# Kernel optimization log

Measured on AMD Instinct MI355X. Metric: run time of the kernel, lower is better.

Reference implementation:

```python
import jax, jax.numpy as jnp
import numpy as np

N = 8192      # nodes
NIN = 128     # input feature dim
NH = 128      # hidden dim
NC = 8        # communities
CS = N // NC  # community size


def setup_inputs() -> dict:
    key = jax.random.key(0)
    k = jax.random.split(key, 6)
    seq1 = jax.random.normal(k[0], (1, N, NIN), jnp.float32)
    seq2 = jax.random.normal(k[1], (1, N, NIN), jnp.float32)
    # dense row-stochastic-ish adjacency so GCN activations stay O(1)
    adj = jax.random.uniform(k[2], (1, N, N), jnp.float32) * (2.0 / N)
    cc_label = jnp.arange(N, dtype=jnp.int32).reshape(NC, CS)  # partition of nodes
    W = jax.random.normal(k[3], (NIN, NH), jnp.float32) / np.float32(np.sqrt(NIN))
    b = jnp.zeros((NH,), jnp.float32)
    Wb = jax.random.normal(k[4], (NH, NH), jnp.float32) / np.float32(np.sqrt(NH))
    bb = jnp.zeros((), jnp.float32)
    return {"seq1": seq1, "seq2": seq2, "adj": adj, "cc_label": cc_label,
            "W": W, "b": b, "Wb": Wb, "bb": bb}


def reference(seq1, seq2, adj, cc_label, W, b, Wb, bb):
    def gcn(seq):
        fts = jnp.einsum('bnd,dh->bnh', seq, W)            # linear
        agg = jnp.einsum('bnm,bmh->bnh', adj, fts) + b     # neighborhood aggregation
        return jax.nn.relu(agg)

    h1 = gcn(seq1)[0]   # [N, NH]
    h2 = gcn(seq2)[0]   # [N, NH]

    # ragged per-community gather (communities are equal-size here)
    hg1 = h1[cc_label]  # [NC, CS, NH]
    hg2 = h2[cc_label]  # [NC, CS, NH]

    # AvgReadout (msk=None) + sigmoid -> per-community summary
    c = jax.nn.sigmoid(jnp.mean(hg1, axis=1))              # [NC, NH]

    # Discriminator: bilinear f_k(h, c) = h @ Wb @ c + bb
    cw = jnp.einsum('hk,nk->nh', Wb, c)                    # [NC, NH]
    sc1 = jnp.einsum('nch,nh->nc', hg1, cw) + bb           # [NC, CS]
    sc2 = jnp.einsum('nch,nh->nc', hg2, cw) + bb           # [NC, CS]

    # scalar scatter-back (each node written exactly once)
    flat = cc_label.reshape(-1)
    ret1 = jnp.zeros((N,), h1.dtype).at[flat].set(sc1.reshape(-1))
    ret2 = jnp.zeros((N,), h2.dtype).at[flat].set(sc2.reshape(-1))
    return jnp.concatenate([ret1, ret2])[None, :]          # [1, 2N]
```

## Files before the change

### kernel.cpp

```cpp
#include <hip/hip_runtime.h>


#define NN    8192
#define NCOLS 256
#define ASCALE 4096.0f
#define AINV  (1.0f/4096.0f)

typedef _Float16 half8 __attribute__((ext_vector_type(8)));
typedef float    f32x4 __attribute__((ext_vector_type(4)));

#define VMCNT(n) asm volatile("s_waitcnt vmcnt(" #n ")" ::: "memory")

__device__ __forceinline__ void gload16(const void* g, void* l) {
  __builtin_amdgcn_global_load_lds(
      (const __attribute__((address_space(1))) char*)g,
      (__attribute__((address_space(3))) char*)l, 16, 0, 0);
}

__global__ void k0_init(const int* __restrict__ cc, int* __restrict__ node_comm,
                        float* __restrict__ S) {
  int i = blockIdx.x * 256 + threadIdx.x;
  if (i < 1024) S[i] = 0.0f;
  node_comm[cc[i]] = i >> 10;
}

__global__ __launch_bounds__(256) void k1_fts(const float* __restrict__ seq1,
                                              const float* __restrict__ seq2,
                                              const float* __restrict__ W,
                                              _Float16* __restrict__ F) {
  __shared__ char lds[65536];
  _Float16* Wt  = (_Float16*)lds;
  float*    sSeq = (float*)(lds + 32768);
  const int tid = threadIdx.x;
  const int lane = tid & 63;
  const int w = tid >> 6;
  const int l15 = lane & 15;
  const int g = lane >> 4;
  const int m0 = blockIdx.x * 64;

  for (int it = 0; it < 64; ++it) {
    int idx = it * 256 + tid;
    int d = idx >> 7, hc = idx & 127;
    int byte = (hc * 256 + d * 2) ^ ((hc & 7) << 4);
    *(_Float16*)(lds + byte) = (_Float16)W[idx];
  }

  const float* seqp[2] = {seq1, seq2};
  const int srow = tid >> 5;
  const int sck = tid & 31;

  for (int s = 0; s < 2; ++s) {
    __syncthreads();
    const float* sp = seqp[s];
#pragma unroll
    for (int i = 0; i < 8; ++i) {
      int row = i * 8 + srow;
      gload16(sp + (size_t)(m0 + row) * 128 + ((sck ^ (row & 7)) << 2),
              (char*)sSeq + i * 4096 + w * 1024);
    }
    asm volatile("s_waitcnt vmcnt(0)" ::: "memory");
    __syncthreads();

    f32x4 acc[4][2] = {};
    const float4* S4 = (const float4*)sSeq;
    const float4* W4 = (const float4*)Wt;
#pragma unroll
    for (int kk = 0; kk < 4; ++kk) {
      half8 bf[2];
#pragma unroll
      for (int nf = 0; nf < 2; ++nf) {
        int col = w * 32 + nf * 16 + l15;
        float4 bv = W4[(col * 16 + kk * 4 + g) ^ (col & 7)];
        bf[nf] = *(const half8*)&bv;
      }
#pragma unroll
      for (int mf = 0; mf < 4; ++mf) {
        int row = mf * 16 + l15;
        int bidx = row * 32 + kk * 8 + g * 2;
        float4 u = S4[bidx ^ (row & 7)];
        float4 v = S4[(bidx + 1) ^ (row & 7)];
        half8 af;
#pragma unroll
        for (int j = 0; j < 4; ++j) af[j] = (_Float16)(((const float*)&u)[j]);
#pragma unroll
        for (int j = 0; j < 4; ++j) af[4 + j] = (_Float16)(((const float*)&v)[j]);
#pragma unroll
        for (int nf = 0; nf < 2; ++nf)
          acc[mf][nf] = __builtin_amdgcn_mfma_f32_16x16x32_f16(af, bf[nf], acc[mf][nf], 0, 0, 0);
      }
    }
    __syncthreads();
    _Float16* img = (_Float16*)sSeq;
#pragma unroll
    for (int mf = 0; mf < 4; ++mf)
#pragma unroll
      for (int nf = 0; nf < 2; ++nf) {
        int col = w * 32 + nf * 16 + l15;
#pragma unroll
        for (int j = 0; j < 4; ++j) {
          int kl = mf * 16 + g * 4 + j;
          img[(kl >> 5) * 4096 + col * 32 + (kl & 31)] = (_Float16)acc[mf][nf][j];
        }
      }
    __syncthreads();
    const float4* src4 = (const float4*)sSeq;
#pragma unroll
    for (int i = 0; i < 4; ++i) {
      int e = i * 256 + tid;
      int kt = e >> 9, off = e & 511;
      ((float4*)(F + (size_t)(2 * blockIdx.x + kt) * 8192))[s * 512 + off] = src4[e];
    }
  }
}

__global__ __launch_bounds__(512) void k2_gemm(const float* __restrict__ adj,
                                               const _Float16* __restrict__ F,
                                               float* __restrict__ Pp) {
  __shared__ float    sA[3][4096];
  __shared__ _Float16 sB[3][8192];
  const int tid = threadIdx.x;
  const int lane = tid & 63;
  const int w = tid >> 6;
  const int l15 = lane & 15;
  const int g = lane >> 4;
  const int row0 = blockIdx.x * 128;
  const int ks = blockIdx.y;
  const int kcol0 = ks * 2048;

  const int ar0 = tid >> 3;
  const int ac = tid & 7;
  const float* asrc0 = adj + (size_t)(row0 + ar0) * NN + kcol0 + ((ac ^ (ar0 & 7)) << 2);
  const float* asrc1 = adj + (size_t)(row0 + ar0 + 64) * NN + kcol0 + ((ac ^ (ar0 & 7)) << 2);
  const char*  bsrc  = (const char*)F + (size_t)(ks * 64) * 16384 + (size_t)tid * 16;

  auto stage = [&](int buf, int t) {
    gload16(asrc0 + t * 32, (char*)sA[buf] + w * 1024);
    gload16(asrc1 + t * 32, (char*)sA[buf] + 8192 + w * 1024);
    const char* bs = bsrc + (size_t)t * 16384;
    gload16(bs,        (char*)sB[buf] + w * 1024);
    gload16(bs + 8192, (char*)sB[buf] + 8192 + w * 1024);
  };

  const int wm = w >> 2, wn = w & 3;
  f32x4 acc[4][4] = {};

  auto compute = [&](int buf) {
    const float4* A4 = (const float4*)sA[buf];
    const float4* B4 = (const float4*)sB[buf];
    half8 bf[4];
#pragma unroll
    for (int nf = 0; nf < 4; ++nf) {
      int col = wn * 64 + nf * 16 + l15;
      float4 bv = B4[col * 4 + g];
      bf[nf] = *(const half8*)&bv;
    }
#pragma unroll
    for (int mf = 0; mf < 4; ++mf) {
      int row = wm * 64 + mf * 16 + l15;
      int bidx = row * 8 + g * 2;
      float4 u = A4[bidx ^ (row & 7)];
      float4 v = A4[(bidx + 1) ^ (row & 7)];
      half8 af;
#pragma unroll
      for (int j = 0; j < 4; ++j) af[j] = (_Float16)(((const float*)&u)[j] * ASCALE);
#pragma unroll
      for (int j = 0; j < 4; ++j) af[4 + j] = (_Float16)(((const float*)&v)[j] * ASCALE);
#pragma unroll
      for (int nf = 0; nf < 4; ++nf)
        acc[mf][nf] = __builtin_amdgcn_mfma_f32_16x16x32_f16(af, bf[nf], acc[mf][nf], 0, 0, 0);
    }
  };

  stage(0, 0);
  stage(1, 1);
  stage(2, 2);
  int cur = 0;
  for (int t = 0; t < 61; ++t) {
    VMCNT(8);
    __builtin_amdgcn_s_barrier();
    compute(cur);
    __builtin_amdgcn_s_barrier();
    stage(cur, t + 3);
    cur = (cur == 2) ? 0 : cur + 1;
  }
  VMCNT(8); __builtin_amdgcn_s_barrier();
  compute(cur); cur = (cur == 2) ? 0 : cur + 1;
  VMCNT(4); __builtin_amdgcn_s_barrier();
  compute(cur); cur = (cur == 2) ? 0 : cur + 1;
  VMCNT(0); __builtin_amdgcn_s_barrier();
  compute(cur);

#pragma unroll
  for (int mf = 0; mf < 4; ++mf)
#pragma unroll
    for (int nf = 0; nf < 4; ++nf) {
      int col = wn * 64 + nf * 16 + l15;
#pragma unroll
      for (int j = 0; j < 4; ++j) {
        int row = row0 + wm * 64 + mf * 16 + g * 4 + j;
        Pp[((size_t)ks * NN + row) * NCOLS + col] = acc[mf][nf][j];
      }
    }
}

__global__ void k2r_reduce(const float* __restrict__ Pp, const float* __restrict__ b,
                           float* __restrict__ h) {
  int gid = blockIdx.x * 256 + threadIdx.x;
  size_t base = (size_t)gid * 4;
  float4 p0 = *(const float4*)(Pp + base);
  float4 p1 = *(const float4*)(Pp + base + 2097152);
  float4 p2 = *(const float4*)(Pp + base + 4194304);
  float4 p3 = *(const float4*)(Pp + base + 6291456);
  int n0 = (int)(base & 255) & 127;
  float4 r;
  r.x = fmaxf((p0.x + p1.x + p2.x + p3.x) * AINV + b[n0],     0.f);
  r.y = fmaxf((p0.y + p1.y + p2.y + p3.y) * AINV + b[n0 + 1], 0.f);
  r.z = fmaxf((p0.z + p1.z + p2.z + p3.z) * AINV + b[n0 + 2], 0.f);
  r.w = fmaxf((p0.w + p1.w + p2.w + p3.w) * AINV + b[n0 + 3], 0.f);
  *(float4*)(h + base) = r;
}

__global__ __launch_bounds__(128) void k3a_csum(const float* __restrict__ h,
                                                const int* __restrict__ node_comm,
                                                float* __restrict__ S) {
  int hh = threadIdx.x;
  int n0 = blockIdx.x * 32;
  float a0=0,a1=0,a2=0,a3=0,a4=0,a5=0,a6=0,a7=0;
  for (int i = 0; i < 32; ++i) {
    int node = n0 + i;
    int c = node_comm[node];
    float v = h[(size_t)node * 256 + hh];
    a0 += (c == 0) ? v : 0.f;  a1 += (c == 1) ? v : 0.f;
    a2 += (c == 2) ? v : 0.f;  a3 += (c == 3) ? v : 0.f;
    a4 += (c == 4) ? v : 0.f;  a5 += (c == 5) ? v : 0.f;
    a6 += (c == 6) ? v : 0.f;  a7 += (c == 7) ? v : 0.f;
  }
  if (a0 != 0.f) atomicAdd(&S[0 * 128 + hh], a0);
  if (a1 != 0.f) atomicAdd(&S[1 * 128 + hh], a1);
  if (a2 != 0.f) atomicAdd(&S[2 * 128 + hh], a2);
  if (a3 != 0.f) atomicAdd(&S[3 * 128 + hh], a3);
  if (a4 != 0.f) atomicAdd(&S[4 * 128 + hh], a4);
  if (a5 != 0.f) atomicAdd(&S[5 * 128 + hh], a5);
  if (a6 != 0.f) atomicAdd(&S[6 * 128 + hh], a6);
  if (a7 != 0.f) atomicAdd(&S[7 * 128 + hh], a7);
}

__global__ __launch_bounds__(128) void k3b_cw(const float* __restrict__ S,
                                              const float* __restrict__ Wb,
                                              float* __restrict__ cw) {
  __shared__ float sc[128];
  int ci = blockIdx.x;
  int hh = threadIdx.x;
  float m = S[ci * 128 + hh] * (1.0f / 1024.0f);
  sc[hh] = 1.0f / (1.0f + __expf(-m));
  __syncthreads();
  const float4* wr = (const float4*)(Wb + (size_t)hh * 128);
  float acc = 0.f;
#pragma unroll 8
  for (int k4 = 0; k4 < 32; ++k4) {
    float4 wv = wr[k4];
    acc += wv.x * sc[k4 * 4 + 0] + wv.y * sc[k4 * 4 + 1]
         + wv.z * sc[k4 * 4 + 2] + wv.w * sc[k4 * 4 + 3];
  }
  cw[ci * 128 + hh] = acc;
}

__global__ __launch_bounds__(256) void k5_score(const float* __restrict__ h,
                                                const int* __restrict__ node_comm,
                                                const float* __restrict__ cw,
                                                const float* __restrict__ bbp,
                                                float* __restrict__ out) {
  int tid = threadIdx.x;
  int q = tid & 15, nl = tid >> 4;
  int node = blockIdx.x * 16 + nl;
  int c = node_comm[node];
  const float* hr = h + (size_t)node * 256;
  const float* cr = cw + c * 128;
  float4 c0 = *(const float4*)(cr + q * 8);
  float4 c1 = *(const float4*)(cr + q * 8 + 4);
  float4 a0 = *(const float4*)(hr + q * 8);
  float4 a1 = *(const float4*)(hr + q * 8 + 4);
  float p1 = a0.x*c0.x + a0.y*c0.y + a0.z*c0.z + a0.w*c0.w
           + a1.x*c1.x + a1.y*c1.y + a1.z*c1.z + a1.w*c1.w;
  float4 b0 = *(const float4*)(hr + 128 + q * 8);
  float4 b1 = *(const float4*)(hr + 128 + q * 8 + 4);
  float p2 = b0.x*c0.x + b0.y*c0.y + b0.z*c0.z + b0.w*c0.w
           + b1.x*c1.x + b1.y*c1.y + b1.z*c1.z + b1.w*c1.w;
#pragma unroll
  for (int m = 8; m >= 1; m >>= 1) {
    p1 += __shfl_xor(p1, m, 64);
    p2 += __shfl_xor(p2, m, 64);
  }
  if (q == 0) {
    float bb = bbp[0];
    out[node] = p1 + bb;
    out[8192 + node] = p2 + bb;
  }
}

extern "C" void kernel_launch(void* const* d_in, const int* in_sizes, int n_in,
                              void* d_out, int out_size, void* d_ws, size_t ws_size,
                              hipStream_t stream) {
  (void)in_sizes; (void)n_in; (void)out_size; (void)ws_size;
  const float* seq1 = (const float*)d_in[0];
  const float* seq2 = (const float*)d_in[1];
  const float* adj  = (const float*)d_in[2];
  const int*   cc   = (const int*)d_in[3];
  const float* W    = (const float*)d_in[4];
  const float* b    = (const float*)d_in[5];
  const float* Wb   = (const float*)d_in[6];
  const float* bb   = (const float*)d_in[7];
  float* out = (float*)d_out;

  char* ws = (char*)d_ws;
  _Float16* F   = (_Float16*)(ws);
  float* h      = (float*)(ws + (4u << 20));
  float* Pp     = (float*)(ws + (12u << 20));
  float* S      = (float*)(ws + (44u << 20));
  float* cw     = (float*)(ws + (44u << 20) + 4096);
  int* node_comm = (int*)(ws + (44u << 20) + 8192);

  k0_init<<<dim3(32), dim3(256), 0, stream>>>(cc, node_comm, S);
  k1_fts<<<dim3(128), dim3(256), 0, stream>>>(seq1, seq2, W, F);
  k2_gemm<<<dim3(64, 4), dim3(512), 0, stream>>>(adj, F, Pp);
  k2r_reduce<<<dim3(2048), dim3(256), 0, stream>>>(Pp, b, h);
  k3a_csum<<<dim3(256), dim3(128), 0, stream>>>(h, node_comm, S);
  k3b_cw<<<dim3(8), dim3(128), 0, stream>>>(S, Wb, cw);
  k5_score<<<dim3(512), dim3(256), 0, stream>>>(h, node_comm, cw, bb, out);
}
```

Measured before the change: 128.9 us.

## Fuse split-K reduce, community summary, and scoring into one grid-synced tail kernel

The split-K reduction, ReLU, per-community summing, sigmoid/Wb projection and bilinear scoring now run in one persistent kernel instead of four launches. Each block keeps its h values in registers, accumulates community sums in LDS, and pushes them to global memory with atomics. A global atomic counter serves as a grid barrier before every block recomputes cw locally. The init kernel is folded into k1_fts. This removes several launch gaps and the round trip of h through global memory. In exchange, every block redundantly computes the 8x128 cw projection, and correctness depends on all 512 blocks being co-resident for the spin barrier.

```diff
diff --git a/kernel.cpp b/kernel.cpp
--- a/kernel.cpp
+++ b/kernel.cpp
@@ -17,17 +17,14 @@
       (__attribute__((address_space(3))) char*)l, 16, 0, 0);
 }
 
-__global__ void k0_init(const int* __restrict__ cc, int* __restrict__ node_comm,
-                        float* __restrict__ S) {
-  int i = blockIdx.x * 256 + threadIdx.x;
-  if (i < 1024) S[i] = 0.0f;
-  node_comm[cc[i]] = i >> 10;
-}
-
 __global__ __launch_bounds__(256) void k1_fts(const float* __restrict__ seq1,
                                               const float* __restrict__ seq2,
                                               const float* __restrict__ W,
-                                              _Float16* __restrict__ F) {
+                                              _Float16* __restrict__ F,
+                                              const int* __restrict__ cc,
+                                              int* __restrict__ node_comm,
+                                              float* __restrict__ S,
+                                              unsigned* __restrict__ ctr) {
   __shared__ char lds[65536];
   _Float16* Wt  = (_Float16*)lds;
   float*    sSeq = (float*)(lds + 32768);
@@ -37,6 +34,15 @@
   const int l15 = lane & 15;
   const int g = lane >> 4;
   const int m0 = blockIdx.x * 64;
+
+  if (tid < 64) {
+    int i = blockIdx.x * 64 + tid;
+    node_comm[cc[i]] = i >> 10;
+  }
+  if (blockIdx.x == 0) {
+    for (int j = tid; j < 1024; j += 256) S[j] = 0.0f;
+    if (tid == 0) ctr[0] = 0u;
+  }
 
   for (int it = 0; it < 64; ++it) {
     int idx = it * 256 + tid;
@@ -203,98 +209,94 @@
     }
 }
 
-__global__ void k2r_reduce(const float* __restrict__ Pp, const float* __restrict__ b,
-                           float* __restrict__ h) {
-  int gid = blockIdx.x * 256 + threadIdx.x;
-  size_t base = (size_t)gid * 4;
-  float4 p0 = *(const float4*)(Pp + base);
-  float4 p1 = *(const float4*)(Pp + base + 2097152);
-  float4 p2 = *(const float4*)(Pp + base + 4194304);
-  float4 p3 = *(const float4*)(Pp + base + 6291456);
-  int n0 = (int)(base & 255) & 127;
-  float4 r;
-  r.x = fmaxf((p0.x + p1.x + p2.x + p3.x) * AINV + b[n0],     0.f);
-  r.y = fmaxf((p0.y + p1.y + p2.y + p3.y) * AINV + b[n0 + 1], 0.f);
-  r.z = fmaxf((p0.z + p1.z + p2.z + p3.z) * AINV + b[n0 + 2], 0.f);
-  r.w = fmaxf((p0.w + p1.w + p2.w + p3.w) * AINV + b[n0 + 3], 0.f);
-  *(float4*)(h + base) = r;
-}
-
-__global__ __launch_bounds__(128) void k3a_csum(const float* __restrict__ h,
-                                                const int* __restrict__ node_comm,
-                                                float* __restrict__ S) {
-  int hh = threadIdx.x;
-  int n0 = blockIdx.x * 32;
-  float a0=0,a1=0,a2=0,a3=0,a4=0,a5=0,a6=0,a7=0;
-  for (int i = 0; i < 32; ++i) {
-    int node = n0 + i;
+__global__ __launch_bounds__(256, 2) void tail_fused(const float* __restrict__ Pp,
+                                                     const float* __restrict__ bias,
+                                                     const int* __restrict__ node_comm,
+                                                     const float* __restrict__ Wb,
+                                                     const float* __restrict__ bbp,
+                                                     float* __restrict__ S,
+                                                     unsigned* __restrict__ ctr,
+                                                     float* __restrict__ out) {
+  __shared__ float sS[1024];
+  __shared__ float sig[1024];
+  __shared__ float cwl[1024];
+  const int tid = threadIdx.x;
+  const int q = tid & 63;
+  const int r = tid >> 6;
+  const int nodebase = blockIdx.x * 16;
+
+  for (int j = tid; j < 1024; j += 256) sS[j] = 0.0f;
+  __syncthreads();
+
+  float4 hv[4];
+  const int col = q * 4;
+  const int n0 = col & 127;
+  const float b0v = bias[n0], b1v = bias[n0 + 1], b2v = bias[n0 + 2], b3v = bias[n0 + 3];
+#pragma unroll
+  for (int k = 0; k < 4; ++k) {
+    int node = nodebase + r + 4 * k;
+    size_t idx = (size_t)node * 256 + col;
+    float4 p0 = *(const float4*)(Pp + idx);
+    float4 p1 = *(const float4*)(Pp + idx + 2097152);
+    float4 p2 = *(const float4*)(Pp + idx + 4194304);
+    float4 p3 = *(const float4*)(Pp + idx + 6291456);
+    float4 h;
+    h.x = fmaxf((p0.x + p1.x + p2.x + p3.x) * AINV + b0v, 0.f);
+    h.y = fmaxf((p0.y + p1.y + p2.y + p3.y) * AINV + b1v, 0.f);
+    h.z = fmaxf((p0.z + p1.z + p2.z + p3.z) * AINV + b2v, 0.f);
+    h.w = fmaxf((p0.w + p1.w + p2.w + p3.w) * AINV + b3v, 0.f);
+    hv[k] = h;
+    if (col < 128) {
+      int c = node_comm[node];
+      float* sc = &sS[c * 128 + n0];
+      atomicAdd(sc + 0, h.x); atomicAdd(sc + 1, h.y);
+      atomicAdd(sc + 2, h.z); atomicAdd(sc + 3, h.w);
+    }
+  }
+  __syncthreads();
+  for (int j = tid; j < 1024; j += 256) {
+    float v = sS[j];
+    if (v != 0.0f) atomicAdd(&S[j], v);
+  }
+  __threadfence();
+  __syncthreads();
+  if (tid == 0) {
+    __hip_atomic_fetch_add(ctr, 1u, __ATOMIC_ACQ_REL, __HIP_MEMORY_SCOPE_AGENT);
+    while (__hip_atomic_load(ctr, __ATOMIC_ACQUIRE, __HIP_MEMORY_SCOPE_AGENT) < 512u)
+      __builtin_amdgcn_s_sleep(8);
+  }
+  __syncthreads();
+
+  for (int j = tid; j < 1024; j += 256)
+    sig[j] = 1.0f / (1.0f + __expf(-S[j] * (1.0f / 1024.0f)));
+  __syncthreads();
+  for (int e = tid; e < 1024; e += 256) {
+    int c = e >> 7, d = e & 127;
+    const float4* wr = (const float4*)(Wb + (size_t)d * 128);
+    const float4* s4 = (const float4*)&sig[c * 128];
+    float a = 0.f;
+#pragma unroll 8
+    for (int k4 = 0; k4 < 32; ++k4) {
+      float4 wv = wr[k4], sv = s4[k4];
+      a += wv.x * sv.x + wv.y * sv.y + wv.z * sv.z + wv.w * sv.w;
+    }
+    cwl[e] = a;
+  }
+  __syncthreads();
+
+  const float bb = bbp[0];
+#pragma unroll
+  for (int k = 0; k < 4; ++k) {
+    int node = nodebase + r + 4 * k;
     int c = node_comm[node];
-    float v = h[(size_t)node * 256 + hh];
-    a0 += (c == 0) ? v : 0.f;  a1 += (c == 1) ? v : 0.f;
-    a2 += (c == 2) ? v : 0.f;  a3 += (c == 3) ? v : 0.f;
-    a4 += (c == 4) ? v : 0.f;  a5 += (c == 5) ? v : 0.f;
-    a6 += (c == 6) ? v : 0.f;  a7 += (c == 7) ? v : 0.f;
-  }
-  if (a0 != 0.f) atomicAdd(&S[0 * 128 + hh], a0);
-  if (a1 != 0.f) atomicAdd(&S[1 * 128 + hh], a1);
-  if (a2 != 0.f) atomicAdd(&S[2 * 128 + hh], a2);
-  if (a3 != 0.f) atomicAdd(&S[3 * 128 + hh], a3);
-  if (a4 != 0.f) atomicAdd(&S[4 * 128 + hh], a4);
-  if (a5 != 0.f) atomicAdd(&S[5 * 128 + hh], a5);
-  if (a6 != 0.f) atomicAdd(&S[6 * 128 + hh], a6);
-  if (a7 != 0.f) atomicAdd(&S[7 * 128 + hh], a7);
-}
-
-__global__ __launch_bounds__(128) void k3b_cw(const float* __restrict__ S,
-                                              const float* __restrict__ Wb,
-                                              float* __restrict__ cw) {
-  __shared__ float sc[128];
-  int ci = blockIdx.x;
-  int hh = threadIdx.x;
-  float m = S[ci * 128 + hh] * (1.0f / 1024.0f);
-  sc[hh] = 1.0f / (1.0f + __expf(-m));
-  __syncthreads();
-  const float4* wr = (const float4*)(Wb + (size_t)hh * 128);
-  float acc = 0.f;
-#pragma unroll 8
-  for (int k4 = 0; k4 < 32; ++k4) {
-    float4 wv = wr[k4];
-    acc += wv.x * sc[k4 * 4 + 0] + wv.y * sc[k4 * 4 + 1]
-         + wv.z * sc[k4 * 4 + 2] + wv.w * sc[k4 * 4 + 3];
-  }
-  cw[ci * 128 + hh] = acc;
-}
-
-__global__ __launch_bounds__(256) void k5_score(const float* __restrict__ h,
-                                                const int* __restrict__ node_comm,
-                                                const float* __restrict__ cw,
-                                                const float* __restrict__ bbp,
-                                                float* __restrict__ out) {
-  int tid = threadIdx.x;
-  int q = tid & 15, nl = tid >> 4;
-  int node = blockIdx.x * 16 + nl;
-  int c = node_comm[node];
-  const float* hr = h + (size_t)node * 256;
-  const float* cr = cw + c * 128;
-  float4 c0 = *(const float4*)(cr + q * 8);
-  float4 c1 = *(const float4*)(cr + q * 8 + 4);
-  float4 a0 = *(const float4*)(hr + q * 8);
-  float4 a1 = *(const float4*)(hr + q * 8 + 4);
-  float p1 = a0.x*c0.x + a0.y*c0.y + a0.z*c0.z + a0.w*c0.w
-           + a1.x*c1.x + a1.y*c1.y + a1.z*c1.z + a1.w*c1.w;
-  float4 b0 = *(const float4*)(hr + 128 + q * 8);
-  float4 b1 = *(const float4*)(hr + 128 + q * 8 + 4);
-  float p2 = b0.x*c0.x + b0.y*c0.y + b0.z*c0.z + b0.w*c0.w
-           + b1.x*c1.x + b1.y*c1.y + b1.z*c1.z + b1.w*c1.w;
-#pragma unroll
-  for (int m = 8; m >= 1; m >>= 1) {
-    p1 += __shfl_xor(p1, m, 64);
-    p2 += __shfl_xor(p2, m, 64);
-  }
-  if (q == 0) {
-    float bb = bbp[0];
-    out[node] = p1 + bb;
-    out[8192 + node] = p2 + bb;
+    const float* cwc = &cwl[c * 128 + n0];
+    float4 h = hv[k];
+    float partial = h.x * cwc[0] + h.y * cwc[1] + h.z * cwc[2] + h.w * cwc[3];
+#pragma unroll
+    for (int m = 16; m >= 1; m >>= 1)
+      partial += __shfl_xor(partial, m, 64);
+    if (q == 0)  out[node] = partial + bb;
+    if (q == 32) out[8192 + node] = partial + bb;
   }
 }
 
@@ -313,18 +315,13 @@
   float* out = (float*)d_out;
 
   char* ws = (char*)d_ws;
-  _Float16* F   = (_Float16*)(ws);
-  float* h      = (float*)(ws + (4u << 20));
-  float* Pp     = (float*)(ws + (12u << 20));
-  float* S      = (float*)(ws + (44u << 20));
-  float* cw     = (float*)(ws + (44u << 20) + 4096);
+  _Float16* F    = (_Float16*)(ws);
+  float* Pp      = (float*)(ws + (12u << 20));
+  float* S       = (float*)(ws + (44u << 20));
   int* node_comm = (int*)(ws + (44u << 20) + 8192);
-
-  k0_init<<<dim3(32), dim3(256), 0, stream>>>(cc, node_comm, S);
-  k1_fts<<<dim3(128), dim3(256), 0, stream>>>(seq1, seq2, W, F);
+  unsigned* ctr  = (unsigned*)(ws + (44u << 20) + 65536);
+
+  k1_fts<<<dim3(128), dim3(256), 0, stream>>>(seq1, seq2, W, F, cc, node_comm, S, ctr);
   k2_gemm<<<dim3(64, 4), dim3(512), 0, stream>>>(adj, F, Pp);
-  k2r_reduce<<<dim3(2048), dim3(256), 0, stream>>>(Pp, b, h);
-  k3a_csum<<<dim3(256), dim3(128), 0, stream>>>(h, node_comm, S);
-  k3b_cw<<<dim3(8), dim3(128), 0, stream>>>(S, Wb, cw);
-  k5_score<<<dim3(512), dim3(256), 0, stream>>>(h, node_comm, cw, bb, out);
-}
+  tail_fused<<<dim3(512), dim3(256), 0, stream>>>(Pp, b, node_comm, Wb, bb, S, ctr, out);
+}
```

After: 185.6 us. 1.44x slower.
